# Kernel optimization log

Hardware: AMD Instinct MI355X
Metric: run time of the kernel (lower is better)

Reference implementation:

```python
import jax, jax.numpy as jnp
import numpy as np

B, G, P, C = 16, 14, 16, 3          # batch, patch grid (14x14), patch size, channels
D, DI, HM, L = 384, 768, 1536, 12   # embed_dim, d_inner=expand*D, mlp_hidden=4*D, depth


def _ln(x, g, b, eps=1e-5):
    m = x.mean(-1, keepdims=True)
    v = ((x - m) ** 2).mean(-1, keepdims=True)
    return (x - m) * jax.lax.rsqrt(v + eps) * g + b


def _lin_attn(seq, wi, bi, wo, bo, g, b):
    # LinearAttention fallback: gated pointwise MLP (SiLU(z)*sigmoid(gate)) + LN + proj_out
    zg = seq @ wi + bi
    z, gate = jnp.split(zg, 2, axis=-1)
    z = jax.nn.silu(z) * jax.nn.sigmoid(gate)
    return _ln(z, g, b) @ wo + bo


def setup_inputs():
    key = jax.random.key(0)
    ks = jax.random.split(key, 8)
    def w(k, shape, s=0.02):
        return (jax.random.normal(k, shape) * s).astype(jnp.float32)
    return {
        'x': jax.random.normal(ks[0], (B, C, G * P, G * P), jnp.float32),
        'patch_w': w(ks[1], (C * P * P, D)), 'patch_b': jnp.zeros((D,), jnp.float32),
        'pe_g': jnp.ones((D,), jnp.float32), 'pe_b': jnp.zeros((D,), jnp.float32),
        'pos': w(ks[2], (1, G * G, D)),
        'n1_g': jnp.ones((L, D), jnp.float32), 'n1_b': jnp.zeros((L, D), jnp.float32),
        'pi_w': w(ks[3], (L, 4, D, 2 * DI)), 'pi_b': jnp.zeros((L, 4, 2 * DI), jnp.float32),
        'po_w': w(ks[4], (L, 4, DI, D)), 'po_b': jnp.zeros((L, 4, D), jnp.float32),
        'la_g': jnp.ones((L, 4, DI), jnp.float32), 'la_b': jnp.zeros((L, 4, DI), jnp.float32),
        'mg_w': w(ks[5], (L, 4 * D, D)), 'mg_b': jnp.zeros((L, D), jnp.float32),
        'sn_g': jnp.ones((L, D), jnp.float32), 'sn_b': jnp.zeros((L, D), jnp.float32),
        'n2_g': jnp.ones((L, D), jnp.float32), 'n2_b': jnp.zeros((L, D), jnp.float32),
        'm1_w': w(ks[6], (L, D, HM)), 'm1_b': jnp.zeros((L, HM), jnp.float32),
        'm2_w': w(ks[7], (L, HM, D)), 'm2_b': jnp.zeros((L, D), jnp.float32),
        'fin_g': jnp.ones((D,), jnp.float32), 'fin_b': jnp.zeros((D,), jnp.float32),
    }


def reference(x, patch_w, patch_b, pe_g, pe_b, pos, n1_g, n1_b, pi_w, pi_b, po_w, po_b,
              la_g, la_b, mg_w, mg_b, sn_g, sn_b, n2_g, n2_b, m1_w, m1_b, m2_w, m2_b,
              fin_g, fin_b):
    Bsz = x.shape[0]
    # Patch embed: non-overlapping conv == per-patch linear projection
    patches = x.reshape(Bsz, C, G, P, G, P).transpose(0, 2, 4, 1, 3, 5).reshape(Bsz, G, G, C * P * P)
    h = _ln(patches @ patch_w + patch_b, pe_g, pe_b)          # [B, G, G, D]
    h = (h.reshape(Bsz, G * G, D) + pos).reshape(Bsz, G, G, D)  # pos embed (no interp: grid==base)
    for l in range(L):
        hn = _ln(h, n1_g[l], n1_b[l])
        # 4-direction scan sequences (-> <- down up)
        ht = hn.transpose(0, 2, 1, 3)
        seqs = [hn.reshape(Bsz, G * G, D),
                hn[:, ::-1, ::-1].reshape(Bsz, G * G, D),
                ht.reshape(Bsz, G * G, D),
                ht[:, ::-1, ::-1].reshape(Bsz, G * G, D)]
        outs = []
        for i in range(4):
            o = _lin_attn(seqs[i], pi_w[l, i], pi_b[l, i], po_w[l, i], po_b[l, i], la_g[l, i], la_b[l, i])
            if i == 1:
                o = o[:, ::-1]
            elif i == 2:
                o = o.reshape(Bsz, G, G, D).transpose(0, 2, 1, 3).reshape(Bsz, G * G, D)
            elif i == 3:
                o = o[:, ::-1].reshape(Bsz, G, G, D).transpose(0, 2, 1, 3).reshape(Bsz, G * G, D)
            outs.append(o)
        merged = jnp.concatenate(outs, axis=-1) @ mg_w[l] + mg_b[l]
        merged = _ln(merged, sn_g[l], sn_b[l]).reshape(Bsz, G, G, D)
        h = h + merged
        hn2 = _ln(h, n2_g[l], n2_b[l])
        h = h + (jax.nn.gelu(hn2 @ m1_w[l] + m1_b[l], approximate=False) @ m2_w[l] + m2_b[l])
    return _ln(h.reshape(Bsz, G * G, D), fin_g, fin_b)  # dense features [B, N, D]
```

## Files before the change

kernel.cpp:

```cpp
#include <hip/hip_runtime.h>
#include <math.h>

typedef unsigned short u16;
typedef __bf16 bf16x8 __attribute__((ext_vector_type(8)));
typedef float f32x4 __attribute__((ext_vector_type(4)));

#define L_   12
#define NTOK 3136
#define MP   3200

__device__ __forceinline__ float b2f(u16 v){ return __builtin_bit_cast(float, (unsigned)v<<16); }
__device__ __forceinline__ u16 f2b(float f){
    unsigned u = __builtin_bit_cast(unsigned, f);
    u += 0x7fffu + ((u>>16)&1u);
    return (u16)(u>>16);
}
__device__ __forceinline__ float wsum(float v){
    #pragma unroll
    for (int o=32;o;o>>=1) v += __shfl_xor(v,o);
    return v;
}
__device__ __forceinline__ void gl_lds16(const void* g, void* l){
    __builtin_amdgcn_global_load_lds(
        (const __attribute__((address_space(1))) void*)g,
        (__attribute__((address_space(3))) void*)l, 16, 0, 0);
}

__device__ __host__ __forceinline__ int rho16(int c){
    return (c < 768) ? (((c>>4)<<5) + (c&15)) : ((((c-768)>>4)<<5) + 16 + ((c-768)&15));
}

__global__ __launch_bounds__(256) void k_transpose(const float* __restrict__ src,
                                                   u16* __restrict__ dst, int R, int C){
    __shared__ float t[32][33];
    long long base = (long long)blockIdx.z * R * C;
    int c0 = blockIdx.x<<5, r0 = blockIdx.y<<5;
    int tx = threadIdx.x & 31, ty = threadIdx.x >> 5;
    #pragma unroll
    for (int i=0;i<32;i+=8)
        t[ty+i][tx] = src[base + (long long)(r0+ty+i)*C + c0 + tx];
    __syncthreads();
    #pragma unroll
    for (int i=0;i<32;i+=8)
        dst[base + (long long)(c0+ty+i)*R + r0 + tx] = f2b(t[tx][ty+i]);
}

__global__ __launch_bounds__(256) void k_transpose_pi(const float* __restrict__ src,
                                                      u16* __restrict__ dst){
    const int R = 384, C = 1536;
    __shared__ float t[32][33];
    long long base = (long long)blockIdx.z * R * C;
    int c0 = blockIdx.x<<5, r0 = blockIdx.y<<5;
    int tx = threadIdx.x & 31, ty = threadIdx.x >> 5;
    #pragma unroll
    for (int i=0;i<32;i+=8)
        t[ty+i][tx] = src[base + (long long)(r0+ty+i)*C + c0 + tx];
    __syncthreads();
    #pragma unroll
    for (int i=0;i<32;i+=8){
        int c = c0 + ty + i;
        dst[base + (long long)rho16(c)*R + r0 + tx] = f2b(t[tx][ty+i]);
    }
}

__global__ __launch_bounds__(256) void k_bi(const float* __restrict__ pi_b, float* __restrict__ out){
    int idx = blockIdx.x*256 + threadIdx.x;
    if (idx >= 48*1536) return;
    int slab = idx / 1536, c = idx - slab*1536;
    int l = slab >> 2, dir = slab & 3;
    out[(long long)l*6144 + dir*1536 + rho16(c)] = pi_b[idx];
}

__global__ __launch_bounds__(256) void k_cvt_g(const float4* __restrict__ src,
                                               const float* __restrict__ la_g,
                                               ushort4* __restrict__ dst){
    int i = blockIdx.x*256 + threadIdx.x;
    if (i >= 3538944) return;
    int flat = i*4;
    int z = flat / 294912, rem = flat - z*294912;
    int ci = rem / 384;
    float gsc = la_g[(long long)z*768 + ci];
    float4 v = src[i];
    ushort4 o; o.x=f2b(v.x*gsc); o.y=f2b(v.y*gsc); o.z=f2b(v.z*gsc); o.w=f2b(v.w*gsc);
    dst[i] = o;
}

__global__ __launch_bounds__(384) void k_bw1(const float* __restrict__ la_b,
                                             const float* __restrict__ po_w,
                                             float* __restrict__ tvec){
    int z = blockIdx.x, chunk = blockIdx.y;
    int i = threadIdx.x;
    const float* pw = po_w + (long long)z*294912;
    const float* lb = la_b + (long long)z*768;
    float s = 0.f;
    int c0 = chunk*128;
    for (int ci=c0; ci<c0+128; ci++) s = fmaf(lb[ci], pw[(long long)ci*384 + i], s);
    atomicAdd(tvec + (long long)z*384 + i, s);
}

__global__ __launch_bounds__(384) void k_bw2(const float* __restrict__ tvec,
                                             const float* __restrict__ po_b,
                                             const float* __restrict__ mg_w,
                                             float* __restrict__ fullb){
    int z = blockIdx.x, chunk = blockIdx.y;
    int l = z>>2, dir = z&3;
    int i = threadIdx.x;
    const float* mw = mg_w + (long long)l*589824 + (long long)dir*147456;
    const float* tv = tvec + (long long)z*384;
    const float* pb = po_b + (long long)z*384;
    float s = 0.f;
    int m0 = chunk*64;
    for (int m=m0; m<m0+64; m++) s = fmaf(tv[m]+pb[m], mw[(long long)m*384 + i], s);
    atomicAdd(fullb + (long long)l*384 + i, s);
}

__global__ __launch_bounds__(256) void k_stats(const u16* __restrict__ gated,
                                               float* __restrict__ st){
    int unit = blockIdx.x*4 + (threadIdx.x>>6);
    int lane = threadIdx.x & 63;
    const u16* p = gated + (long long)(unit>>2)*3072 + (unit&3)*768;
    float s1 = 0.f, s2 = 0.f;
    #pragma unroll
    for (int i=0;i<3;i++){
        ushort4 v = *reinterpret_cast<const ushort4*>(p + i*256 + lane*4);
        const u16* a = (const u16*)&v;
        #pragma unroll
        for (int q=0;q<4;q++){ float f = b2f(a[q]); s1 += f; s2 += f*f; }
    }
    s1 = wsum(s1); s2 = wsum(s2);
    if (lane==0){
        st[(long long)unit*2]   = s1;
        st[(long long)unit*2+1] = s2;
    }
}

__global__ __launch_bounds__(256) void k_patches(const float* __restrict__ x, u16* __restrict__ out){
    int idx = blockIdx.x*256 + threadIdx.x;
    int row = idx / 768, col = idx - row*768;
    float v = 0.f;
    if (row < NTOK){
        int b = row / 196, t = row - b*196;
        int gi = t / 14, gj = t - gi*14;
        int c = col >> 8, rem = col & 255, pi = rem >> 4, pj = rem & 15;
        v = x[((long long)(b*3 + c)*224 + gi*16 + pi)*224 + gj*16 + pj];
    }
    out[idx] = f2b(v);
}

template<int EPI, int BM>
__global__ __launch_bounds__(256) void gemm_tn(
    const u16* __restrict__ A, int lda, long long aSh, long long aSl,
    const u16* __restrict__ Bt, int ldb, long long bSh, long long bSl,
    const float* __restrict__ bias, long long biasSh, int splitBias,
    void* __restrict__ Cbase, int ldc, long long cSh, long long cSl,
    int K, int zshift, const float* __restrict__ aux, float* __restrict__ auxw)
{
    constexpr int NF = (BM==128) ? 4 : 2;
    constexpr int AI = (BM==128) ? 4 : 2;
    int z = blockIdx.z;
    int zh = z >> zshift, zl = z - (zh << zshift);
    const u16* Az  = A  + zh*aSh + zl*aSl;
    const u16* Btz = Bt + zh*bSh + zl*bSl;
    bool addb = bias && (!splitBias || zl == 0);
    long long cOff = zh*cSh + zl*cSl;
    int m0 = blockIdx.y*BM, n0 = blockIdx.x*128;

    __shared__ u16 As[2][BM*64];
    __shared__ u16 Bs[2][8192];

    int tid = threadIdx.x;
    int lane = tid & 63;
    int w = tid >> 6;
    int wrb = (BM==128) ? (w>>1)*64 : 0;
    int wcb = (BM==128) ? (w&1)*64 : w*32;
    int rsub = lane >> 3, csub = lane & 7;
    int scol = ((csub ^ rsub) << 3);
    int kxor = (lane & 7) << 4;

    const u16* ga[AI]; const u16* gb[4]; int loa[AI], lob[4];
    #pragma unroll
    for (int j=0;j<AI;j++){
        int r = j*32 + w*8 + rsub;
        ga[j] = Az + (long long)(m0 + r)*lda + scol;
        loa[j] = (j*32 + w*8)*64;
    }
    #pragma unroll
    for (int j=0;j<4;j++){
        int r = j*32 + w*8 + rsub;
        gb[j] = Btz + (long long)(n0 + r)*ldb + scol;
        lob[j] = (j*32 + w*8)*64;
    }

    f32x4 acc[4][NF];
    #pragma unroll
    for (int m=0;m<4;m++)
        #pragma unroll
        for (int n=0;n<NF;n++) acc[m][n] = (f32x4){0.f,0.f,0.f,0.f};

    int nkt = K >> 6;

    auto stage = [&](int ko, int p){
        #pragma unroll
        for (int j=0;j<AI;j++) gl_lds16(ga[j] + ko, &As[p][loa[j]]);
        #pragma unroll
        for (int j=0;j<4;j++)  gl_lds16(gb[j] + ko, &Bs[p][lob[j]]);
    };

    stage(0, 0);
    stage(64, 1);

    auto step = [&](int kt, int p){
        if (kt == nkt-1)               asm volatile("s_waitcnt vmcnt(0)" ::: "memory");
        else if constexpr (BM==128)    asm volatile("s_waitcnt vmcnt(8)" ::: "memory");
        else                           asm volatile("s_waitcnt vmcnt(6)" ::: "memory");
        __builtin_amdgcn_s_barrier();
        const char* as = (const char*)As[p];
        const char* bs = (const char*)Bs[p];
        bf16x8 af[2][4], bfr[2][NF];
        #pragma unroll
        for (int kk=0; kk<2; ++kk){
            int kb = ((kk*32 + ((lane>>4)<<3))*2) ^ kxor;
            #pragma unroll
            for (int m=0;m<4;m++){
                int r = wrb + m*16 + (lane&15);
                af[kk][m] = *reinterpret_cast<const bf16x8*>(as + r*128 + kb);
            }
            #pragma unroll
            for (int n=0;n<NF;n++){
                int r = wcb + n*16 + (lane&15);
                bfr[kk][n] = *reinterpret_cast<const bf16x8*>(bs + r*128 + kb);
            }
        }
        asm volatile("s_waitcnt lgkmcnt(0)" ::: "memory");
        __builtin_amdgcn_sched_barrier(0);
        __builtin_amdgcn_s_barrier();
        if (kt+2 < nkt) stage((kt+2)<<6, p);
        #pragma unroll
        for (int kk=0; kk<2; ++kk)
            #pragma unroll
            for (int m=0;m<4;m++)
                #pragma unroll
                for (int n=0;n<NF;n++)
                    acc[m][n] = __builtin_amdgcn_mfma_f32_16x16x32_bf16(af[kk][m], bfr[kk][n], acc[m][n], 0,0,0);
    };

    for (int kt=0; kt<nkt; kt+=2){ step(kt, 0); step(kt+1, 1); }

    int rbase = m0 + wrb;
    int nbase = n0 + wcb;
    if (EPI==3){
        int dir = n0/1536;
        #pragma unroll
        for (int np2=0; np2<NF/2; ++np2){
            int ncz = nbase + (np2*2)*16 + (lane&15);
            int pz  = ncz - dir*1536;
            int ci  = ((pz>>5)<<4) + (pz&15);
            float bz = addb ? bias[ncz]      : 0.f;
            float bg = addb ? bias[ncz+16]   : 0.f;
            #pragma unroll
            for (int m=0;m<4;m++){
                #pragma unroll
                for (int r4=0;r4<4;r4++){
                    int row = rbase + m*16 + ((lane>>4)<<2) + r4;
                    float vz = acc[m][np2*2][r4]   + bz;
                    float vg = acc[m][np2*2+1][r4] + bg;
                    float gv = vz / ((1.f+__expf(-vz))*(1.f+__expf(-vg)));
                    ((u16*)Cbase)[(long long)row*3072 + dir*768 + ci] = f2b(gv);
                }
            }
        }
    } else if (EPI==4){
        #pragma unroll
        for (int m=0;m<4;m++){
            #pragma unroll
            for (int r4=0;r4<4;r4++){
                int row = rbase + m*16 + ((lane>>4)<<2) + r4;
                float st1 = aux[((long long)row*4 + zl)*2];
                float st2 = aux[((long long)row*4 + zl)*2 + 1];
                float mu = st1*(1.f/768.f);
                float rs = rsqrtf(st2*(1.f/768.f) - mu*mu + 1e-5f);
                #pragma unroll
                for (int n=0;n<NF;n++){
                    int ncol = nbase + n*16 + (lane&15);
                    float gsv = bias[(long long)zl*384 + ncol];
                    ((float*)Cbase)[(long long)row*ldc + ncol + cOff] = (acc[m][n][r4] - mu*gsv)*rs;
                }
            }
        }
    } else if (EPI==5){
        #pragma unroll
        for (int m=0;m<4;m++){
            #pragma unroll
            for (int r4=0;r4<4;r4++){
                int row = rbase + m*16 + ((lane>>4)<<2) + r4;
                float s = 0.f;
                #pragma unroll
                for (int n=0;n<NF;n++){
                    int ncol = nbase + n*16 + (lane&15);
                    u16 rv = f2b(acc[m][n][r4]);
                    ((u16*)Cbase)[(long long)row*ldc + ncol + cOff] = rv;
                    s += b2f(rv);
                }
                #pragma unroll
                for (int o=1;o<16;o<<=1) s += __shfl_xor(s, o);
                if ((lane&15)==0) atomicAdd(auxw + (long long)z*384 + row, s);
            }
        }
    } else {
        #pragma unroll
        for (int m=0;m<4;m++){
            #pragma unroll
            for (int n=0;n<NF;n++){
                int ncol = nbase + n*16 + (lane&15);
                float bv = addb ? bias[zh*biasSh + ncol] : 0.f;
                #pragma unroll
                for (int r4=0;r4<4;r4++){
                    int row = rbase + m*16 + ((lane>>4)<<2) + r4;
                    float v = acc[m][n][r4] + bv;
                    long long idx = (long long)row*ldc + ncol + cOff;
                    if (EPI==0)      ((u16*)Cbase)[idx] = f2b(v);
                    else if (EPI==1){
                        float gl = 0.5f*v*(1.f + erff(v*0.70710678118f));
                        ((u16*)Cbase)[idx] = f2b(gl);
                    }
                    else             ((float*)Cbase)[idx] = v;
                }
            }
        }
    }
}

template<int MODE>
__global__ __launch_bounds__(256) void k_addln(float* __restrict__ h,
        const float* __restrict__ parts, int np,
        const float* __restrict__ g, const float* __restrict__ b, void* __restrict__ out){
    int row = blockIdx.x*4 + (threadIdx.x>>6);
    int lane = threadIdx.x & 63;
    float* hp = h + (long long)row*384;
    float v[6]; float s = 0.f;
    #pragma unroll
    for (int i=0;i<6;i++){
        int c = lane + i*64;
        float t = hp[c];
        for (int p=0;p<np;p++) t += parts[(long long)p*MP*384 + (long long)row*384 + c];
        v[i] = t; s += t;
    }
    if (MODE==0 && np){
        #pragma unroll
        for (int i=0;i<6;i++) hp[lane + i*64] = v[i];
    }
    float mu = wsum(s)*(1.f/384.f);
    float q = 0.f;
    #pragma unroll
    for (int i=0;i<6;i++){ float d = v[i]-mu; q += d*d; }
    float rs = rsqrtf(wsum(q)*(1.f/384.f) + 1e-5f);
    if (MODE==0){
        u16* op = (u16*)out + (long long)row*384;
        #pragma unroll
        for (int i=0;i<6;i++){ int c = lane + i*64; op[c] = f2b((v[i]-mu)*rs*g[c] + b[c]); }
    } else {
        float* op = (float*)out + (long long)row*384;
        #pragma unroll
        for (int i=0;i<6;i++){ int c = lane + i*64; op[c] = (v[i]-mu)*rs*g[c] + b[c]; }
    }
}

__global__ __launch_bounds__(256) void k_pe_ln(const float* __restrict__ parts,
        const float* __restrict__ g, const float* __restrict__ b,
        const float* __restrict__ pos, float* __restrict__ h,
        const float* __restrict__ n1g, const float* __restrict__ n1b,
        u16* __restrict__ hn){
    int row = blockIdx.x*4 + (threadIdx.x>>6);
    int lane = threadIdx.x & 63;
    float v[6]; float s = 0.f;
    #pragma unroll
    for (int i=0;i<6;i++){
        int c = lane + i*64;
        float t = parts[(long long)row*384 + c] + parts[(long long)MP*384 + (long long)row*384 + c];
        v[i] = t; s += t;
    }
    float mu = wsum(s)*(1.f/384.f);
    float q = 0.f;
    #pragma unroll
    for (int i=0;i<6;i++){ float d = v[i]-mu; q += d*d; }
    float rs = rsqrtf(wsum(q)*(1.f/384.f) + 1e-5f);
    int t = row % 196;
    const float* pp = pos + (long long)t*384;
    float* op = h + (long long)row*384;
    float hv[6]; float s2 = 0.f;
    #pragma unroll
    for (int i=0;i<6;i++){
        int c = lane + i*64;
        float nv = (v[i]-mu)*rs*g[c] + b[c] + pp[c];
        op[c] = nv; hv[i] = nv; s2 += nv;
    }
    float mu2 = wsum(s2)*(1.f/384.f);
    float q2 = 0.f;
    #pragma unroll
    for (int i=0;i<6;i++){ float d = hv[i]-mu2; q2 += d*d; }
    float rs2 = rsqrtf(wsum(q2)*(1.f/384.f) + 1e-5f);
    u16* hp = hn + (long long)row*384;
    #pragma unroll
    for (int i=0;i<6;i++){ int c = lane + i*64; hp[c] = f2b((hv[i]-mu2)*rs2*n1g[c] + n1b[c]); }
}

__global__ __launch_bounds__(256) void k_sn_ln(const float* __restrict__ parts,
        const float* __restrict__ fullb, const float* __restrict__ mgb,
        const float* __restrict__ sg, const float* __restrict__ sb,
        float* __restrict__ h,
        const float* __restrict__ n2g, const float* __restrict__ n2b,
        u16* __restrict__ hn2){
    int row = blockIdx.x*4 + (threadIdx.x>>6);
    int lane = threadIdx.x & 63;
    float v[6]; float s = 0.f;
    #pragma unroll
    for (int i=0;i<6;i++){
        int c = lane + i*64;
        long long o = (long long)row*384 + c;
        float t = mgb[c] + fullb[c];
        #pragma unroll
        for (int p=0;p<4;p++) t += parts[(long long)p*MP*384 + o];
        v[i] = t; s += t;
    }
    float mu = wsum(s)*(1.f/384.f);
    float q = 0.f;
    #pragma unroll
    for (int i=0;i<6;i++){ float d = v[i]-mu; q += d*d; }
    float rs = rsqrtf(wsum(q)*(1.f/384.f) + 1e-5f);
    float* hp = h + (long long)row*384;
    float hv[6]; float s2 = 0.f;
    #pragma unroll
    for (int i=0;i<6;i++){
        int c = lane + i*64;
        float nv = hp[c] + (v[i]-mu)*rs*sg[c] + sb[c];
        hp[c] = nv; hv[i] = nv; s2 += nv;
    }
    float mu2 = wsum(s2)*(1.f/384.f);
    float q2 = 0.f;
    #pragma unroll
    for (int i=0;i<6;i++){ float d = hv[i]-mu2; q2 += d*d; }
    float rs2 = rsqrtf(wsum(q2)*(1.f/384.f) + 1e-5f);
    u16* op = hn2 + (long long)row*384;
    #pragma unroll
    for (int i=0;i<6;i++){ int c = lane + i*64; op[c] = f2b((hv[i]-mu2)*rs2*n2g[c] + n2b[c]); }
}

extern "C" void kernel_launch(void* const* d_in, const int* in_sizes, int n_in,
                              void* d_out, int out_size, void* d_ws, size_t ws_size,
                              hipStream_t stream)
{
    const float* x      = (const float*)d_in[0];
    const float* patch_w= (const float*)d_in[1];
    const float* patch_b= (const float*)d_in[2];
    const float* pe_g   = (const float*)d_in[3];
    const float* pe_b   = (const float*)d_in[4];
    const float* pos    = (const float*)d_in[5];
    const float* n1_g   = (const float*)d_in[6];
    const float* n1_b   = (const float*)d_in[7];
    const float* pi_w   = (const float*)d_in[8];
    const float* pi_b   = (const float*)d_in[9];
    const float* po_w   = (const float*)d_in[10];
    const float* po_b   = (const float*)d_in[11];
    const float* la_g   = (const float*)d_in[12];
    const float* la_b   = (const float*)d_in[13];
    const float* mg_w   = (const float*)d_in[14];
    const float* mg_b   = (const float*)d_in[15];
    const float* sn_g   = (const float*)d_in[16];
    const float* sn_b   = (const float*)d_in[17];
    const float* n2_g   = (const float*)d_in[18];
    const float* n2_b   = (const float*)d_in[19];
    const float* m1_w   = (const float*)d_in[20];
    const float* m1_b   = (const float*)d_in[21];
    const float* m2_w   = (const float*)d_in[22];
    const float* m2_b   = (const float*)d_in[23];
    const float* fin_g  = (const float*)d_in[24];
    const float* fin_b  = (const float*)d_in[25];

    char* wptr = (char*)d_ws;
    auto carve = [&](long long elems, int esz)->void*{
        void* p = (void*)wptr;
        wptr += ((elems*(long long)esz + 255)/256)*256;
        return p;
    };

    u16* wt_pi  = (u16*)carve(28311552, 2);
    u16* wt_mgr = (u16*)carve(7077888, 2);
    u16* wt_m1  = (u16*)carve(7077888, 2);
    u16* wt_m2  = (u16*)carve(7077888, 2);
    u16* wt_pe  = (u16*)carve(294912, 2);
    u16* po_bf  = (u16*)carve(14155776, 2);
    u16* WcT    = (u16*)carve(14155776, 2);
    float* Gs   = (float*)carve(48*384, 4);
    float* tvec = (float*)carve(48*384, 4);
    float* fullb= (float*)carve(12*384, 4);
    size_t zbytes = (size_t)((char*)(fullb + 12*384) - (char*)Gs);
    float* stats= (float*)carve(MP*8, 4);
    float* pib_i= (float*)carve(12*6144, 4);
    float* h    = (float*)carve((long long)MP*384, 4);
    float* parts= (float*)carve(4LL*MP*384, 4);
    u16* patches= (u16*)carve((long long)MP*768, 2);
    u16* hn     = (u16*)carve((long long)MP*384, 2);
    u16* gated  = (u16*)carve((long long)MP*3072, 2);
    u16* outs   = (u16*)carve((long long)MP*1536, 2);

    dim3 blk(256);

    hipMemsetAsync(Gs, 0, zbytes, stream);
    k_transpose_pi<<<dim3(48,12,48), blk, 0, stream>>>(pi_w, wt_pi);
    k_bi<<<dim3((48*1536+255)/256), blk, 0, stream>>>(pi_b, pib_i);
    k_transpose<<<dim3(12,12,48), blk, 0, stream>>>(mg_w,   wt_mgr, 384, 384);
    k_transpose<<<dim3(48,12,12), blk, 0, stream>>>(m1_w,   wt_m1, 384, 1536);
    k_transpose<<<dim3(12,48,12), blk, 0, stream>>>(m2_w,   wt_m2, 1536, 384);
    k_transpose<<<dim3(12,24,1),  blk, 0, stream>>>(patch_w,wt_pe, 768, 384);
    k_cvt_g<<<dim3(13824), blk, 0, stream>>>((const float4*)po_w, la_g, (ushort4*)po_bf);
    k_bw1<<<dim3(48,6), dim3(384), 0, stream>>>(la_b, po_w, tvec);
    k_bw2<<<dim3(48,6), dim3(384), 0, stream>>>(tvec, po_b, mg_w, fullb);
    gemm_tn<5,128><<<dim3(6,3,48), blk, 0, stream>>>(
        wt_mgr, 384, 589824LL, 147456LL,
        po_bf,  384, 1179648LL, 294912LL,
        nullptr, 0, 0,
        WcT, 3072, 1179648LL, 768LL, 384, 2, nullptr, Gs);

    k_patches<<<dim3(MP*768/256), blk, 0, stream>>>(x, patches);
    gemm_tn<2,64><<<dim3(3,50,2), blk, 0, stream>>>(
        patches, 768, 0, 384,
        wt_pe,   768, 0, 384,
        patch_b, 0, 1,
        parts, 384, 0, (long long)MP*384, 384, 1, nullptr, nullptr);
    k_pe_ln<<<dim3(MP/4), blk, 0, stream>>>(parts, pe_g, pe_b, pos, h, n1_g, n1_b, hn);

    for (int l=0; l<L_; ++l){
        gemm_tn<3,128><<<dim3(48,25,1), blk, 0, stream>>>(
            hn, 384, 0, 0,
            wt_pi + (long long)l*2359296, 384, 0, 0,
            pib_i + (long long)l*6144, 0, 0,
            gated, 3072, 0, 0, 384, 0, nullptr, nullptr);
        k_stats<<<dim3(MP), blk, 0, stream>>>(gated, stats);
        gemm_tn<4,64><<<dim3(3,50,4), blk, 0, stream>>>(
            gated, 3072, 0, 768,
            WcT + (long long)l*1179648, 3072, 0, 768,
            Gs + (long long)l*1536, 0, 0,
            parts, 384, 0, (long long)MP*384, 768, 2, stats, nullptr);
        k_sn_ln<<<dim3(MP/4), blk, 0, stream>>>(parts,
                                                fullb + (long long)l*384, mg_b + l*384,
                                                sn_g + l*384, sn_b + l*384,
                                                h, n2_g + l*384, n2_b + l*384, hn);
        gemm_tn<1,64><<<dim3(12,50,1), blk, 0, stream>>>(
            hn, 384, 0, 0,
            wt_m1 + (long long)l*589824, 384, 0, 0,
            m1_b + (long long)l*1536, 0, 0,
            outs, 1536, 0, 0, 384, 0, nullptr, nullptr);
        gemm_tn<2,64><<<dim3(3,50,2), blk, 0, stream>>>(
            outs, 1536, 0, 768,
            wt_m2 + (long long)l*589824, 1536, 0, 768,
            m2_b + l*384, 0, 1,
            parts, 384, 0, (long long)MP*384, 768, 1, nullptr, nullptr);
        if (l < L_-1)
            k_addln<0><<<dim3(MP/4), blk, 0, stream>>>(h, parts, 2,
                n1_g + (l+1)*384, n1_b + (l+1)*384, hn);
        else
            k_addln<1><<<dim3(NTOK/4), blk, 0, stream>>>(h, parts, 2,
                fin_g, fin_b, (float*)d_out);
    }
}
```

Measured before the change: 1.321 ms.

## Add BN tile parameter, widen pi GEMM tile, split m2 K four ways, fuse weight prep

Makes the GEMM's N tile a template parameter. The per-layer input projection now uses 128x192 tiles (32 column blocks instead of 48), cutting redundant A-tile loads. The MLP down-projection is split along K into four partial sums instead of two, which raises the block count for better CU occupancy, and the add+LN kernel now sums four partials. The weight conversion and bias-fold preprocessing kernels are merged into one pass over po_w. In exchange, the larger tile uses more LDS and registers, and the extra split-K partials add memory traffic.

```diff
diff --git a/kernel.cpp b/kernel.cpp
--- a/kernel.cpp
+++ b/kernel.cpp
@@ -71,30 +71,24 @@
     out[(long long)l*6144 + dir*1536 + rho16(c)] = pi_b[idx];
 }
 
-__global__ __launch_bounds__(256) void k_cvt_g(const float4* __restrict__ src,
-                                               const float* __restrict__ la_g,
-                                               ushort4* __restrict__ dst){
-    int i = blockIdx.x*256 + threadIdx.x;
-    if (i >= 3538944) return;
-    int flat = i*4;
-    int z = flat / 294912, rem = flat - z*294912;
-    int ci = rem / 384;
-    float gsc = la_g[(long long)z*768 + ci];
-    float4 v = src[i];
-    ushort4 o; o.x=f2b(v.x*gsc); o.y=f2b(v.y*gsc); o.z=f2b(v.z*gsc); o.w=f2b(v.w*gsc);
-    dst[i] = o;
-}
-
-__global__ __launch_bounds__(384) void k_bw1(const float* __restrict__ la_b,
-                                             const float* __restrict__ po_w,
-                                             float* __restrict__ tvec){
+__global__ __launch_bounds__(384) void k_cvt_bw(const float* __restrict__ po_w,
+                                                const float* __restrict__ la_g,
+                                                const float* __restrict__ la_b,
+                                                u16* __restrict__ po_bf,
+                                                float* __restrict__ tvec){
     int z = blockIdx.x, chunk = blockIdx.y;
     int i = threadIdx.x;
     const float* pw = po_w + (long long)z*294912;
+    u16* ob = po_bf + (long long)z*294912;
     const float* lb = la_b + (long long)z*768;
+    const float* lg = la_g + (long long)z*768;
     float s = 0.f;
     int c0 = chunk*128;
-    for (int ci=c0; ci<c0+128; ci++) s = fmaf(lb[ci], pw[(long long)ci*384 + i], s);
+    for (int ci=c0; ci<c0+128; ci++){
+        float v = pw[(long long)ci*384 + i];
+        s = fmaf(lb[ci], v, s);
+        ob[(long long)ci*384 + i] = f2b(v * lg[ci]);
+    }
     atomicAdd(tvec + (long long)z*384 + i, s);
 }
 
@@ -147,7 +141,7 @@
     out[idx] = f2b(v);
 }
 
-template<int EPI, int BM>
+template<int EPI, int BM, int BN>
 __global__ __launch_bounds__(256) void gemm_tn(
     const u16* __restrict__ A, int lda, long long aSh, long long aSl,
     const u16* __restrict__ Bt, int ldb, long long bSh, long long bSl,
@@ -155,29 +149,31 @@
     void* __restrict__ Cbase, int ldc, long long cSh, long long cSl,
     int K, int zshift, const float* __restrict__ aux, float* __restrict__ auxw)
 {
-    constexpr int NF = (BM==128) ? 4 : 2;
-    constexpr int AI = (BM==128) ? 4 : 2;
+    constexpr int AI = BM/32;
+    constexpr int BI = BN/32;
+    constexpr int NF = (BM==128) ? BN/32 : BN/64;
+    constexpr int LP = AI + BI;
     int z = blockIdx.z;
     int zh = z >> zshift, zl = z - (zh << zshift);
     const u16* Az  = A  + zh*aSh + zl*aSl;
     const u16* Btz = Bt + zh*bSh + zl*bSl;
     bool addb = bias && (!splitBias || zl == 0);
     long long cOff = zh*cSh + zl*cSl;
-    int m0 = blockIdx.y*BM, n0 = blockIdx.x*128;
+    int m0 = blockIdx.y*BM, n0 = blockIdx.x*BN;
 
     __shared__ u16 As[2][BM*64];
-    __shared__ u16 Bs[2][8192];
+    __shared__ u16 Bs[2][BN*64];
 
     int tid = threadIdx.x;
     int lane = tid & 63;
     int w = tid >> 6;
     int wrb = (BM==128) ? (w>>1)*64 : 0;
-    int wcb = (BM==128) ? (w&1)*64 : w*32;
+    int wcb = (BM==128) ? (w&1)*(BN/2) : w*(BN/4);
     int rsub = lane >> 3, csub = lane & 7;
     int scol = ((csub ^ rsub) << 3);
     int kxor = (lane & 7) << 4;
 
-    const u16* ga[AI]; const u16* gb[4]; int loa[AI], lob[4];
+    const u16* ga[AI]; const u16* gb[BI]; int loa[AI], lob[BI];
     #pragma unroll
     for (int j=0;j<AI;j++){
         int r = j*32 + w*8 + rsub;
@@ -185,7 +181,7 @@
         loa[j] = (j*32 + w*8)*64;
     }
     #pragma unroll
-    for (int j=0;j<4;j++){
+    for (int j=0;j<BI;j++){
         int r = j*32 + w*8 + rsub;
         gb[j] = Btz + (long long)(n0 + r)*ldb + scol;
         lob[j] = (j*32 + w*8)*64;
@@ -203,16 +199,17 @@
         #pragma unroll
         for (int j=0;j<AI;j++) gl_lds16(ga[j] + ko, &As[p][loa[j]]);
         #pragma unroll
-        for (int j=0;j<4;j++)  gl_lds16(gb[j] + ko, &Bs[p][lob[j]]);
+        for (int j=0;j<BI;j++) gl_lds16(gb[j] + ko, &Bs[p][lob[j]]);
     };
 
     stage(0, 0);
     stage(64, 1);
 
     auto step = [&](int kt, int p){
-        if (kt == nkt-1)               asm volatile("s_waitcnt vmcnt(0)" ::: "memory");
-        else if constexpr (BM==128)    asm volatile("s_waitcnt vmcnt(8)" ::: "memory");
-        else                           asm volatile("s_waitcnt vmcnt(6)" ::: "memory");
+        if (kt == nkt-1)            asm volatile("s_waitcnt vmcnt(0)" ::: "memory");
+        else if constexpr (LP==6)   asm volatile("s_waitcnt vmcnt(6)" ::: "memory");
+        else if constexpr (LP==8)   asm volatile("s_waitcnt vmcnt(8)" ::: "memory");
+        else                        asm volatile("s_waitcnt vmcnt(10)" ::: "memory");
         __builtin_amdgcn_s_barrier();
         const char* as = (const char*)As[p];
         const char* bs = (const char*)Bs[p];
@@ -512,17 +509,16 @@
     k_transpose<<<dim3(48,12,12), blk, 0, stream>>>(m1_w,   wt_m1, 384, 1536);
     k_transpose<<<dim3(12,48,12), blk, 0, stream>>>(m2_w,   wt_m2, 1536, 384);
     k_transpose<<<dim3(12,24,1),  blk, 0, stream>>>(patch_w,wt_pe, 768, 384);
-    k_cvt_g<<<dim3(13824), blk, 0, stream>>>((const float4*)po_w, la_g, (ushort4*)po_bf);
-    k_bw1<<<dim3(48,6), dim3(384), 0, stream>>>(la_b, po_w, tvec);
+    k_cvt_bw<<<dim3(48,6), dim3(384), 0, stream>>>(po_w, la_g, la_b, po_bf, tvec);
     k_bw2<<<dim3(48,6), dim3(384), 0, stream>>>(tvec, po_b, mg_w, fullb);
-    gemm_tn<5,128><<<dim3(6,3,48), blk, 0, stream>>>(
+    gemm_tn<5,128,128><<<dim3(6,3,48), blk, 0, stream>>>(
         wt_mgr, 384, 589824LL, 147456LL,
         po_bf,  384, 1179648LL, 294912LL,
         nullptr, 0, 0,
         WcT, 3072, 1179648LL, 768LL, 384, 2, nullptr, Gs);
 
     k_patches<<<dim3(MP*768/256), blk, 0, stream>>>(x, patches);
-    gemm_tn<2,64><<<dim3(3,50,2), blk, 0, stream>>>(
+    gemm_tn<2,64,128><<<dim3(3,50,2), blk, 0, stream>>>(
         patches, 768, 0, 384,
         wt_pe,   768, 0, 384,
         patch_b, 0, 1,
@@ -530,13 +526,13 @@
     k_pe_ln<<<dim3(MP/4), blk, 0, stream>>>(parts, pe_g, pe_b, pos, h, n1_g, n1_b, hn);
 
     for (int l=0; l<L_; ++l){
-        gemm_tn<3,128><<<dim3(48,25,1), blk, 0, stream>>>(
+        gemm_tn<3,128,192><<<dim3(32,25,1), blk, 0, stream>>>(
             hn, 384, 0, 0,
             wt_pi + (long long)l*2359296, 384, 0, 0,
             pib_i + (long long)l*6144, 0, 0,
             gated, 3072, 0, 0, 384, 0, nullptr, nullptr);
         k_stats<<<dim3(MP), blk, 0, stream>>>(gated, stats);
-        gemm_tn<4,64><<<dim3(3,50,4), blk, 0, stream>>>(
+        gemm_tn<4,64,128><<<dim3(3,50,4), blk, 0, stream>>>(
             gated, 3072, 0, 768,
             WcT + (long long)l*1179648, 3072, 0, 768,
             Gs + (long long)l*1536, 0, 0,
@@ -545,21 +541,21 @@
                                                 fullb + (long long)l*384, mg_b + l*384,
                                                 sn_g + l*384, sn_b + l*384,
                                                 h, n2_g + l*384, n2_b + l*384, hn);
-        gemm_tn<1,64><<<dim3(12,50,1), blk, 0, stream>>>(
+        gemm_tn<1,64,128><<<dim3(12,50,1), blk, 0, stream>>>(
             hn, 384, 0, 0,
             wt_m1 + (long long)l*589824, 384, 0, 0,
             m1_b + (long long)l*1536, 0, 0,
             outs, 1536, 0, 0, 384, 0, nullptr, nullptr);
-        gemm_tn<2,64><<<dim3(3,50,2), blk, 0, stream>>>(
-            outs, 1536, 0, 768,
-            wt_m2 + (long long)l*589824, 1536, 0, 768,
+        gemm_tn<2,64,128><<<dim3(3,50,4), blk, 0, stream>>>(
+            outs, 1536, 0, 384,
+            wt_m2 + (long long)l*589824, 1536, 0, 384,
             m2_b + l*384, 0, 1,
-            parts, 384, 0, (long long)MP*384, 768, 1, nullptr, nullptr);
+            parts, 384, 0, (long long)MP*384, 384, 2, nullptr, nullptr);
         if (l < L_-1)
-            k_addln<0><<<dim3(MP/4), blk, 0, stream>>>(h, parts, 2,
+            k_addln<0><<<dim3(MP/4), blk, 0, stream>>>(h, parts, 4,
                 n1_g + (l+1)*384, n1_b + (l+1)*384, hn);
         else
-            k_addln<1><<<dim3(NTOK/4), blk, 0, stream>>>(h, parts, 2,
+            k_addln<1><<<dim3(NTOK/4), blk, 0, stream>>>(h, parts, 4,
                 fin_g, fin_b, (float*)d_out);
     }
 }
```

Measured after the change: 1.473 ms. 1.12x slower.
